# Kernel tuning notes

Measured on AMD Instinct MI355X. Metric: run time of the kernel, lower is better.

## Reference

```python
import jax, jax.numpy as jnp
import numpy as np

B, S, D, L, R = 8, 128, 512, 512, 50  # batch, seq_len, input_dim, linear_dim, n_rel_labels


def _head_params(key, n_out):
    k1, k2, k3, k4 = jax.random.split(key, 4)
    s1 = 1.0 / np.sqrt(2 * D)
    s2 = 1.0 / np.sqrt(L)
    return (jax.random.uniform(k1, (2 * D, L), jnp.float32, -s1, s1),
            jax.random.uniform(k2, (L,), jnp.float32, -s1, s1),
            jax.random.uniform(k3, (L, n_out), jnp.float32, -s2, s2),
            jax.random.uniform(k4, (n_out,), jnp.float32, -s2, s2))


def setup_inputs() -> dict:
    key = jax.random.key(0)
    kx, ks, kh, kt, kl = jax.random.split(key, 5)
    x = jax.random.normal(kx, (B, S, D), jnp.float32)
    span = _head_params(ks, 1)
    h2h = _head_params(kh, 1)
    t2t = _head_params(kt, 1)
    lab = _head_params(kl, R)
    return {
        'x': x,
        'span_W1': span[0], 'span_b1': span[1], 'span_W2': span[2], 'span_b2': span[3],
        'h2h_W1': h2h[0], 'h2h_b1': h2h[1], 'h2h_W2': h2h[2], 'h2h_b2': h2h[3],
        't2t_W1': t2t[0], 't2t_b1': t2t[1], 't2t_W2': t2t[2], 't2t_b2': t2t[3],
        'lab_W1': lab[0], 'lab_b1': lab[1], 'lab_W2': lab[2], 'lab_b2': lab[3],
    }


def _pair_head(x, W1, b1, W2, b2):
    # Linear on concat([x_i, x_j]) == x_i @ W_left + x_j @ W_right  (avoids [B,S,S,2D] concat)
    d = x.shape[-1]
    Wl, Wr = W1[:d], W1[d:]
    left = jnp.einsum('bid,dl->bil', x, Wl)   # [B,S,L]
    right = jnp.einsum('bjd,dl->bjl', x, Wr)  # [B,S,L]
    h = jnp.tanh(left[:, :, None, :] + right[:, None, :, :] + b1)  # [B,S,S,L]
    return jnp.einsum('bijl,lo->bijo', h, W2) + b2  # [B,S,S,n_out]


def reference(x, span_W1, span_b1, span_W2, span_b2,
              h2h_W1, h2h_b1, h2h_W2, h2h_b2,
              t2t_W1, t2t_b1, t2t_W2, t2t_b2,
              lab_W1, lab_b1, lab_W2, lab_b2):
    shst = _pair_head(x, span_W1, span_b1, span_W2, span_b2)[..., 0]  # [B,S,S]
    # torch: movedim(-1,1) -> triu + triu(1).T -> movedim(1,-1)
    bt = jnp.swapaxes(shst, 1, 2)
    sym = jnp.triu(bt) + jnp.swapaxes(jnp.triu(bt, 1), -1, -2)
    shst = jnp.swapaxes(sym, 1, 2)
    shoh = _pair_head(x, h2h_W1, h2h_b1, h2h_W2, h2h_b2)[..., 0]
    stot = _pair_head(x, t2t_W1, t2t_b1, t2t_W2, t2t_b2)[..., 0]
    shoh_labels = _pair_head(x, lab_W1, lab_b1, lab_W2, lab_b2)  # [B,S,S,R]
    return (shst, shoh, stot, shoh_labels)
```

## Files before the change

kernel.cpp:

```cpp
#include <hip/hip_runtime.h>

#define Bsz 8
#define Ssz 128
#define Dsz 512
#define D2 1024
#define Lsz 512
#define Rsz 50
#define SLOT 524288
#define BSLOT 65536
#define OUTMAT 131072

typedef __attribute__((ext_vector_type(8))) _Float16 f16x8;
typedef __attribute__((ext_vector_type(2))) __fp16 fp16x2;
typedef __attribute__((ext_vector_type(4))) float f32x4;

union UV4 { uint4 u; f16x8 h; };
union UH { unsigned short s; _Float16 h; };
union UP { fp16x2 h; unsigned u; };

struct K1Args {
  const float* W1[4];
  const float* b1[4];
};

__device__ __forceinline__ float f16lo(unsigned u) {
  UH x; x.s = (unsigned short)(u & 0xffffu); return (float)x.h;
}
__device__ __forceinline__ float f16hi(unsigned u) {
  UH x; x.s = (unsigned short)(u >> 16); return (float)x.h;
}
__device__ __forceinline__ unsigned pkrtz(float a, float b) {
  UP c; c.h = __builtin_amdgcn_cvt_pkrtz(a, b); return c.u;
}
__device__ __forceinline__ unsigned short f2h(float v) {
  UH x; x.h = (_Float16)v; return x.s;
}
__device__ __forceinline__ float rcpf(float x) {
  return __builtin_amdgcn_rcpf(x);
}

__global__ __launch_bounds__(256) void prep_all(
    const float* __restrict__ x, K1Args a, const float* __restrict__ W2,
    unsigned short* __restrict__ W1F, unsigned short* __restrict__ X16F,
    unsigned short* __restrict__ W2F) {
  const int z = blockIdx.z;
  const int t = threadIdx.x;
  if (z < 4) {
    if (blockIdx.x >= 8) return;
    __shared__ float S[64][65];
    const float* __restrict__ W = a.W1[z];
    const int n0 = blockIdx.x * 64;
    const int k0 = blockIdx.y * 64;
    {
      const int kk = t >> 2, c16 = (t & 3) * 16;
      const float* p = W + (k0 + kk) * Lsz + n0 + c16;
#pragma unroll
      for (int c = 0; c < 4; ++c) {
        float4 v = *(const float4*)(p + c * 4);
        S[kk][c16 + c * 4 + 0] = v.x; S[kk][c16 + c * 4 + 1] = v.y;
        S[kk][c16 + c * 4 + 2] = v.z; S[kk][c16 + c * 4 + 3] = v.w;
      }
    }
    __syncthreads();
#pragma unroll
    for (int o = t; o < 512; o += 256) {
      const int lane = o & 63;
      const int ntl = (o >> 6) & 3, kbl = o >> 8;
      const int n_l = ntl * 16 + (lane & 15);
      const int k_l = kbl * 32 + (lane >> 4) * 8;
      uint4 pk;
      pk.x = pkrtz(S[k_l + 0][n_l], S[k_l + 1][n_l]);
      pk.y = pkrtz(S[k_l + 2][n_l], S[k_l + 3][n_l]);
      pk.z = pkrtz(S[k_l + 4][n_l], S[k_l + 5][n_l]);
      pk.w = pkrtz(S[k_l + 6][n_l], S[k_l + 7][n_l]);
      const long addr =
          ((long)((z * 32 + blockIdx.x * 4 + ntl) * 32 + blockIdx.y * 2 + kbl) *
               64 + lane) * 8;
      *(uint4*)(W1F + addr) = pk;
    }
  } else if (z == 4) {
    const int idx = (blockIdx.y * 16 + blockIdx.x) * 256 + t;
    const int frag = idx >> 6, lane = idx & 63;
    const int m = (frag >> 4) * 16 + (lane & 15);
    const int k0 = (frag & 15) * 32 + (lane >> 4) * 8;
    const float* p = x + m * Dsz + k0;
    float4 v0 = *(const float4*)p, v1 = *(const float4*)(p + 4);
    uint4 pk = make_uint4(pkrtz(v0.x, v0.y), pkrtz(v0.z, v0.w),
                          pkrtz(v1.x, v1.y), pkrtz(v1.z, v1.w));
    *(uint4*)(X16F + (long)idx * 8) = pk;
  } else {
    if (blockIdx.y != 0 || blockIdx.x >= 16) return;
    const int idx = blockIdx.x * 256 + t;
    const int frag = idx >> 6, lane = idx & 63;
    const int o = (frag >> 4) * 16 + (lane & 15);
    const int k0 = (frag & 15) * 32 + (lane >> 4) * 8;
    float v[8];
#pragma unroll
    for (int e = 0; e < 8; ++e)
      v[e] = (o < Rsz) ? W2[(k0 + e) * Rsz + o] : 0.0f;
    uint4 pk = make_uint4(pkrtz(v[0], v[1]), pkrtz(v[2], v[3]),
                          pkrtz(v[4], v[5]), pkrtz(v[6], v[7]));
    *(uint4*)(W2F + (long)idx * 8) = pk;
  }
}

__global__ __launch_bounds__(256) void gemm_lr_f16f(
    const unsigned short* __restrict__ X16F,
    const unsigned short* __restrict__ W1F, K1Args a,
    unsigned short* __restrict__ U) {
  const int side = blockIdx.z;
  const int h = side >> 1, r = side & 1;
  const float* __restrict__ bias = a.b1[h];
  const int tid = threadIdx.x;
  const int w = tid >> 6, lane = tid & 63;
  const int lm = lane & 15, q = lane >> 4;
  const int mtb = blockIdx.y * 4 + (w & 1) * 2;
  const int ntb = blockIdx.x * 4 + (w >> 1) * 2;

  f32x4 acc[2][2];
#pragma unroll
  for (int mt = 0; mt < 2; ++mt)
#pragma unroll
    for (int nt = 0; nt < 2; ++nt) {
      acc[mt][nt].x = 0.f; acc[mt][nt].y = 0.f;
      acc[mt][nt].z = 0.f; acc[mt][nt].w = 0.f;
    }

  for (int kb = 0; kb < 16; ++kb) {
    UV4 af[2], bf[2];
#pragma unroll
    for (int mt = 0; mt < 2; ++mt)
      af[mt].u = *(const uint4*)(X16F +
          ((long)((mtb + mt) * 16 + kb) * 64 + lane) * 8);
#pragma unroll
    for (int nt = 0; nt < 2; ++nt)
      bf[nt].u = *(const uint4*)(W1F +
          ((long)((h * 32 + ntb + nt) * 32 + r * 16 + kb) * 64 + lane) * 8);
#pragma unroll
    for (int mt = 0; mt < 2; ++mt)
#pragma unroll
      for (int nt = 0; nt < 2; ++nt)
        acc[mt][nt] = __builtin_amdgcn_mfma_f32_16x16x32_f16(
            af[mt].h, bf[nt].h, acc[mt][nt], 0, 0, 0);
  }

  unsigned short* slot = U + side * SLOT;
  if (h < 3) {
#pragma unroll
    for (int nt = 0; nt < 2; ++nt) {
      const int n_out = (ntb + nt) * 16 + lm;
      const float bb = (r == 0) ? bias[n_out] : 0.0f;
#pragma unroll
      for (int mt = 0; mt < 2; ++mt) {
        const int m0r = (mtb + mt) * 16 + q * 4;
        const float e0 = __expf(2.0f * (acc[mt][nt].x + bb));
        const float e1 = __expf(2.0f * (acc[mt][nt].y + bb));
        const float e2 = __expf(2.0f * (acc[mt][nt].z + bb));
        const float e3 = __expf(2.0f * (acc[mt][nt].w + bb));
        uint2 pr;
        pr.x = pkrtz(e0, e1);
        pr.y = pkrtz(e2, e3);
        const int bi = m0r >> 7, il = m0r & 127;
        *(uint2*)(slot + bi * BSLOT + n_out * Ssz + il) = pr;
      }
    }
  } else {
#pragma unroll
    for (int nt = 0; nt < 2; ++nt) {
      const int n_out = (ntb + nt) * 16 + lm;
      const float bb = (r == 0) ? bias[n_out] : 0.0f;
#pragma unroll
      for (int mt = 0; mt < 2; ++mt) {
#pragma unroll
        for (int reg = 0; reg < 4; ++reg) {
          const int m_out = (mtb + mt) * 16 + q * 4 + reg;
          float v;
          if (reg == 0) v = acc[mt][nt].x;
          else if (reg == 1) v = acc[mt][nt].y;
          else if (reg == 2) v = acc[mt][nt].z;
          else v = acc[mt][nt].w;
          slot[m_out * Lsz + n_out] = f2h(__expf(2.0f * (v + bb)));
        }
      }
    }
  }
}

__global__ __launch_bounds__(256) void pair_scalar5(
    const unsigned short* __restrict__ U,
    const float* __restrict__ w2a, const float* __restrict__ w2b,
    const float* __restrict__ w2c, float* __restrict__ P) {
  const int zh = blockIdx.z;
  const int h = zh >> 1, half = zh & 1;
  const int b = blockIdx.y;
  const int it = blockIdx.x >> 2, jt = blockIdx.x & 3;
  if (h == 0 && jt > it) return;
  const int i0 = it * 32, j0 = jt * 32;
  const int t = threadIdx.x;
  const int tj = t & 15, ti = t >> 4;

  const unsigned short* __restrict__ A  = U + (2 * h) * SLOT + b * BSLOT;
  const unsigned short* __restrict__ Bt = U + (2 * h + 1) * SLOT + b * BSLOT;
  const float* __restrict__ w2 = (h == 0) ? w2a : (h == 1 ? w2b : w2c);

  __shared__ unsigned short Ls[64][40];
  __shared__ unsigned short Rs[64][40];
  __shared__ float w2s[64];

  float acc00 = 0.f, acc01 = 0.f, acc10 = 0.f, acc11 = 0.f;
  const int sr = t >> 2;
  const int sc = (t & 3) * 8;
  const int lbase = half * 256;

  for (int lc = 0; lc < 256; lc += 64) {
    __syncthreads();
    const int gl = lbase + lc + sr;
    *(uint4*)&Ls[sr][sc] = *(const uint4*)(A + gl * Ssz + i0 + sc);
    *(uint4*)&Rs[sr][sc] = *(const uint4*)(Bt + gl * Ssz + j0 + sc);
    if (t < 64) w2s[t] = w2[lbase + lc + t];
    __syncthreads();
#pragma unroll 4
    for (int l = 0; l < 64; ++l) {
      const unsigned ua = *(const unsigned*)&Ls[l][ti * 2];
      const unsigned ub = *(const unsigned*)&Rs[l][tj * 2];
      const float ax = f16lo(ua), ay = f16hi(ua);
      const float bx = f16lo(ub), by = f16hi(ub);
      const float wv = w2s[l];
      acc00 = fmaf(wv, rcpf(fmaf(ax, bx, 1.0f)), acc00);
      acc01 = fmaf(wv, rcpf(fmaf(ax, by, 1.0f)), acc01);
      acc10 = fmaf(wv, rcpf(fmaf(ay, bx, 1.0f)), acc10);
      acc11 = fmaf(wv, rcpf(fmaf(ay, by, 1.0f)), acc11);
    }
  }

  float* Pp = P + ((long)(zh * Bsz + b)) * 16384;
  const int i = i0 + ti * 2, j = j0 + tj * 2;
  *(float2*)&Pp[(i + 0) * Ssz + j] = make_float2(acc00, acc01);
  *(float2*)&Pp[(i + 1) * Ssz + j] = make_float2(acc10, acc11);
}

__global__ __launch_bounds__(128) void combine_scalar(
    const float* __restrict__ P,
    const float* __restrict__ w2a, const float* __restrict__ w2b,
    const float* __restrict__ w2c,
    const float* __restrict__ b2a, const float* __restrict__ b2b,
    const float* __restrict__ b2c,
    float* __restrict__ out) {
  const int h = blockIdx.z;
  const int b = blockIdx.y;
  const int i = blockIdx.x;
  const int t = threadIdx.x;
  const float* __restrict__ w2 = (h == 0) ? w2a : (h == 1 ? w2b : w2c);
  const float bias = (h == 0) ? b2a[0] : (h == 1 ? b2b[0] : b2c[0]);

  __shared__ float red[128];
  float s = w2[t] + w2[t + 128] + w2[t + 256] + w2[t + 384];
  red[t] = s;
  __syncthreads();
  if (t < 64) red[t] += red[t + 64];
  __syncthreads();
  if (t < 32) red[t] += red[t + 32];
  __syncthreads();
  if (t < 16) red[t] += red[t + 16];
  __syncthreads();
  if (t < 8) red[t] += red[t + 8];
  __syncthreads();
  if (t < 4) red[t] += red[t + 4];
  __syncthreads();
  if (t < 2) red[t] += red[t + 2];
  __syncthreads();
  const float S = red[0] + red[1];

  const float* P0 = P + ((long)(h * 2 * Bsz + b)) * 16384;
  const float* P1 = P + ((long)((h * 2 + 1) * Bsz + b)) * 16384;
  int ii = i, jj = t;
  if (h == 0 && t > i) { ii = t; jj = i; }
  const float p = P0[ii * Ssz + jj] + P1[ii * Ssz + jj];
  out[h * OUTMAT + (b * Ssz + i) * Ssz + t] = S - 2.0f * p + bias;
}

__global__ __launch_bounds__(256) void pair_label7(
    const unsigned short* __restrict__ U,
    const unsigned short* __restrict__ W2F,
    const float* __restrict__ b2, float* __restrict__ out) {
  const int b = blockIdx.z;
  const int i = blockIdx.x;
  const int tid = threadIdx.x;
  const int w = tid >> 6, lane = tid & 63;
  const int lm = lane & 15, q = lane >> 4;
  const int jb = blockIdx.y * 64 + w * 16;

  const unsigned short* __restrict__ L0 = U + 6 * SLOT + (b * Ssz + i) * Lsz;
  const unsigned short* __restrict__ Rr = U + 7 * SLOT + (b * Ssz + jb + lm) * Lsz;
  float* out3 = out + 3 * OUTMAT;

  f32x4 acc[4];
#pragma unroll
  for (int nt = 0; nt < 4; ++nt) {
    acc[nt].x = 0.f; acc[nt].y = 0.f;
    acc[nt].z = 0.f; acc[nt].w = 0.f;
  }

  const int kq = q * 8;
  uint4 rc  = *(const uint4*)(Rr + kq);
  uint4 l0c = *(const uint4*)(L0 + kq);

#pragma unroll 1
  for (int kc = 0; kc < Lsz; kc += 32) {
    const int kn = ((kc + 32) & 511) + kq;
    uint4 rn  = *(const uint4*)(Rr + kn);
    uint4 l0n = *(const uint4*)(L0 + kn);
    UV4 bf[4];
    const int kb = kc >> 5;
#pragma unroll
    for (int nt = 0; nt < 4; ++nt)
      bf[nt].u = *(const uint4*)(W2F + ((long)(nt * 16 + kb) * 64 + lane) * 8);

    float rf[8] = {f16lo(rc.x), f16hi(rc.x), f16lo(rc.y), f16hi(rc.y),
                   f16lo(rc.z), f16hi(rc.z), f16lo(rc.w), f16hi(rc.w)};
    float a0[8] = {f16lo(l0c.x), f16hi(l0c.x), f16lo(l0c.y), f16hi(l0c.y),
                   f16lo(l0c.z), f16hi(l0c.z), f16lo(l0c.w), f16hi(l0c.w)};
    float h0[8];
#pragma unroll
    for (int e = 0; e < 8; ++e)
      h0[e] = fmaf(-2.0f, rcpf(fmaf(a0[e], rf[e], 1.0f)), 1.0f);
    UV4 A0;
    A0.u = make_uint4(pkrtz(h0[0], h0[1]), pkrtz(h0[2], h0[3]),
                      pkrtz(h0[4], h0[5]), pkrtz(h0[6], h0[7]));
#pragma unroll
    for (int nt = 0; nt < 4; ++nt)
      acc[nt] = __builtin_amdgcn_mfma_f32_16x16x32_f16(
          A0.h, bf[nt].h, acc[nt], 0, 0, 0);
    rc = rn; l0c = l0n;
  }

#pragma unroll
  for (int nt = 0; nt < 4; ++nt) {
    const int o = nt * 16 + lm;
    if (o >= Rsz) continue;
    const float bias = b2[o];
#pragma unroll
    for (int reg = 0; reg < 4; ++reg) {
      const int j = jb + q * 4 + reg;
      const long base = ((long)((b * Ssz + i) * Ssz) + j) * Rsz;
      float v;
      if (reg == 0) v = acc[nt].x;
      else if (reg == 1) v = acc[nt].y;
      else if (reg == 2) v = acc[nt].z;
      else v = acc[nt].w;
      out3[base + o] = v + bias;
    }
  }
}

extern "C" void kernel_launch(void* const* d_in, const int* in_sizes, int n_in,
                              void* d_out, int out_size, void* d_ws,
                              size_t ws_size, hipStream_t stream) {
  (void)in_sizes; (void)n_in; (void)out_size; (void)ws_size;
  const float* x = (const float*)d_in[0];
  K1Args a;
  a.W1[0] = (const float*)d_in[1];  a.b1[0] = (const float*)d_in[2];
  a.W1[1] = (const float*)d_in[5];  a.b1[1] = (const float*)d_in[6];
  a.W1[2] = (const float*)d_in[9];  a.b1[2] = (const float*)d_in[10];
  a.W1[3] = (const float*)d_in[13]; a.b1[3] = (const float*)d_in[14];
  const float* w2a = (const float*)d_in[3];
  const float* b2a = (const float*)d_in[4];
  const float* w2b = (const float*)d_in[7];
  const float* b2b = (const float*)d_in[8];
  const float* w2c = (const float*)d_in[11];
  const float* b2c = (const float*)d_in[12];
  const float* W2l = (const float*)d_in[15];
  const float* b2l = (const float*)d_in[16];
  float* out = (float*)d_out;

  unsigned short* U    = (unsigned short*)d_ws;
  unsigned short* W1F  = U + 8 * SLOT;
  unsigned short* X16F = U + 8 * SLOT + 4 * (Lsz * D2);
  unsigned short* W2F  = U + 8 * SLOT + 5 * (Lsz * D2);
  float* P = (float*)W1F;

  prep_all<<<dim3(16, 16, 6), 256, 0, stream>>>(x, a, W2l, W1F, X16F, W2F);
  gemm_lr_f16f<<<dim3(8, 16, 8), 256, 0, stream>>>(X16F, W1F, a, U);
  pair_scalar5<<<dim3(16, Bsz, 6), 256, 0, stream>>>(U, w2a, w2b, w2c, P);
  combine_scalar<<<dim3(Ssz, Bsz, 3), 128, 0, stream>>>(
      P, w2a, w2b, w2c, b2a, b2b, b2c, out);
  pair_label7<<<dim3(Ssz, 2, Bsz), 256, 0, stream>>>(U, W2F, b2l, out);
}
```

Measured before the change: 185.3 us.

## Stage right-operand and W2 fragments in double-buffered LDS for label head

The label pair kernel now has each block cover all 128 j positions for one (b,i) row instead of 64, with each wave computing two 16-row M tiles. The right-hand activations and the W2 fragments are loaded cooperatively into double-buffered shared memory, and the next chunk is prefetched while the current one is computed. The aim is to cut redundant global loads of W2 and R rows across waves and blocks. In exchange the grid has half as many blocks, LDS use and register pressure rise, and a barrier is added per k chunk.

```diff
diff --git a/kernel.cpp b/kernel.cpp
--- a/kernel.cpp
+++ b/kernel.cpp
@@ -279,59 +279,113 @@
   out[h * OUTMAT + (b * Ssz + i) * Ssz + t] = S - 2.0f * p + bias;
 }
 
-__global__ __launch_bounds__(256) void pair_label7(
+__global__ __launch_bounds__(256) void pair_label8(
     const unsigned short* __restrict__ U,
     const unsigned short* __restrict__ W2F,
     const float* __restrict__ b2, float* __restrict__ out) {
-  const int b = blockIdx.z;
+  const int b = blockIdx.y;
   const int i = blockIdx.x;
   const int tid = threadIdx.x;
   const int w = tid >> 6, lane = tid & 63;
   const int lm = lane & 15, q = lane >> 4;
-  const int jb = blockIdx.y * 64 + w * 16;
-
-  const unsigned short* __restrict__ L0 = U + 6 * SLOT + (b * Ssz + i) * Lsz;
-  const unsigned short* __restrict__ Rr = U + 7 * SLOT + (b * Ssz + jb + lm) * Lsz;
+  const int jb = w * 32;
+
+  const unsigned short* __restrict__ Lrow = U + 6 * SLOT + (b * Ssz + i) * Lsz;
+  const unsigned short* __restrict__ Rb0 = U + 7 * SLOT + (long)b * Ssz * Lsz;
   float* out3 = out + 3 * OUTMAT;
 
-  f32x4 acc[4];
-#pragma unroll
-  for (int nt = 0; nt < 4; ++nt) {
-    acc[nt].x = 0.f; acc[nt].y = 0.f;
-    acc[nt].z = 0.f; acc[nt].w = 0.f;
-  }
-
-  const int kq = q * 8;
-  uint4 rc  = *(const uint4*)(Rr + kq);
-  uint4 l0c = *(const uint4*)(L0 + kq);
+  __shared__ unsigned short Rs[2][128][68];
+  __shared__ unsigned short Bs[2][8][512];
+
+  const int sr = tid >> 1;
+  const int sh = (tid & 1) * 32;
+  const unsigned short* Rg = Rb0 + sr * Lsz + sh;
+  const int bfrag = tid >> 5;
+  const int bo = (tid & 31) * 16;
+  const int fragN = (bfrag & 3) * 16 + (bfrag >> 2);
+
+  f32x4 acc[2][4];
+#pragma unroll
+  for (int mt = 0; mt < 2; ++mt)
+#pragma unroll
+    for (int nt = 0; nt < 4; ++nt) {
+      acc[mt][nt].x = 0.f; acc[mt][nt].y = 0.f;
+      acc[mt][nt].z = 0.f; acc[mt][nt].w = 0.f;
+    }
+
+  uint4 rp0, rp1, rp2, rp3, bp0, bp1;
+  {
+    const unsigned short* p = Rg;
+    rp0 = *(const uint4*)(p);      rp1 = *(const uint4*)(p + 8);
+    rp2 = *(const uint4*)(p + 16); rp3 = *(const uint4*)(p + 24);
+    const unsigned short* bp = W2F + (long)fragN * 512 + bo;
+    bp0 = *(const uint4*)(bp);     bp1 = *(const uint4*)(bp + 8);
+  }
+  *(uint4*)&Rs[0][sr][sh + 0]  = rp0;
+  *(uint4*)&Rs[0][sr][sh + 8]  = rp1;
+  *(uint4*)&Rs[0][sr][sh + 16] = rp2;
+  *(uint4*)&Rs[0][sr][sh + 24] = rp3;
+  *(uint4*)&Bs[0][bfrag][bo]     = bp0;
+  *(uint4*)&Bs[0][bfrag][bo + 8] = bp1;
+  __syncthreads();
 
 #pragma unroll 1
-  for (int kc = 0; kc < Lsz; kc += 32) {
-    const int kn = ((kc + 32) & 511) + kq;
-    uint4 rn  = *(const uint4*)(Rr + kn);
-    uint4 l0n = *(const uint4*)(L0 + kn);
-    UV4 bf[4];
-    const int kb = kc >> 5;
-#pragma unroll
-    for (int nt = 0; nt < 4; ++nt)
-      bf[nt].u = *(const uint4*)(W2F + ((long)(nt * 16 + kb) * 64 + lane) * 8);
-
-    float rf[8] = {f16lo(rc.x), f16hi(rc.x), f16lo(rc.y), f16hi(rc.y),
-                   f16lo(rc.z), f16hi(rc.z), f16lo(rc.w), f16hi(rc.w)};
-    float a0[8] = {f16lo(l0c.x), f16hi(l0c.x), f16lo(l0c.y), f16hi(l0c.y),
-                   f16lo(l0c.z), f16hi(l0c.z), f16lo(l0c.w), f16hi(l0c.w)};
-    float h0[8];
-#pragma unroll
-    for (int e = 0; e < 8; ++e)
-      h0[e] = fmaf(-2.0f, rcpf(fmaf(a0[e], rf[e], 1.0f)), 1.0f);
-    UV4 A0;
-    A0.u = make_uint4(pkrtz(h0[0], h0[1]), pkrtz(h0[2], h0[3]),
-                      pkrtz(h0[4], h0[5]), pkrtz(h0[6], h0[7]));
-#pragma unroll
-    for (int nt = 0; nt < 4; ++nt)
-      acc[nt] = __builtin_amdgcn_mfma_f32_16x16x32_f16(
-          A0.h, bf[nt].h, acc[nt], 0, 0, 0);
-    rc = rn; l0c = l0n;
+  for (int c = 0; c < 8; ++c) {
+    const int buf = c & 1;
+    if (c < 7) {
+      const unsigned short* p = Rg + (c + 1) * 64;
+      rp0 = *(const uint4*)(p);      rp1 = *(const uint4*)(p + 8);
+      rp2 = *(const uint4*)(p + 16); rp3 = *(const uint4*)(p + 24);
+      const unsigned short* bp = W2F + (long)(fragN + (c + 1) * 2) * 512 + bo;
+      bp0 = *(const uint4*)(bp);     bp1 = *(const uint4*)(bp + 8);
+    }
+    const uint4 lf0 = *(const uint4*)(Lrow + c * 64 + q * 8);
+    const uint4 lf1 = *(const uint4*)(Lrow + c * 64 + 32 + q * 8);
+
+#pragma unroll
+    for (int kbl = 0; kbl < 2; ++kbl) {
+      const uint4 lf = kbl ? lf1 : lf0;
+      float ea[8];
+      ea[0] = f16lo(lf.x); ea[1] = f16hi(lf.x);
+      ea[2] = f16lo(lf.y); ea[3] = f16hi(lf.y);
+      ea[4] = f16lo(lf.z); ea[5] = f16hi(lf.z);
+      ea[6] = f16lo(lf.w); ea[7] = f16hi(lf.w);
+      UV4 bfr[4];
+#pragma unroll
+      for (int nt = 0; nt < 4; ++nt)
+        bfr[nt].u = *(const uint4*)&Bs[buf][kbl * 4 + nt][lane * 8];
+#pragma unroll
+      for (int mt = 0; mt < 2; ++mt) {
+        const uint4 rv =
+            *(const uint4*)&Rs[buf][jb + mt * 16 + lm][kbl * 32 + q * 8];
+        float eb[8];
+        eb[0] = f16lo(rv.x); eb[1] = f16hi(rv.x);
+        eb[2] = f16lo(rv.y); eb[3] = f16hi(rv.y);
+        eb[4] = f16lo(rv.z); eb[5] = f16hi(rv.z);
+        eb[6] = f16lo(rv.w); eb[7] = f16hi(rv.w);
+        float hh[8];
+#pragma unroll
+        for (int e = 0; e < 8; ++e)
+          hh[e] = fmaf(-2.0f, rcpf(fmaf(ea[e], eb[e], 1.0f)), 1.0f);
+        UV4 A;
+        A.u = make_uint4(pkrtz(hh[0], hh[1]), pkrtz(hh[2], hh[3]),
+                         pkrtz(hh[4], hh[5]), pkrtz(hh[6], hh[7]));
+#pragma unroll
+        for (int nt = 0; nt < 4; ++nt)
+          acc[mt][nt] = __builtin_amdgcn_mfma_f32_16x16x32_f16(
+              A.h, bfr[nt].h, acc[mt][nt], 0, 0, 0);
+      }
+    }
+    if (c < 7) {
+      const int nb = buf ^ 1;
+      *(uint4*)&Rs[nb][sr][sh + 0]  = rp0;
+      *(uint4*)&Rs[nb][sr][sh + 8]  = rp1;
+      *(uint4*)&Rs[nb][sr][sh + 16] = rp2;
+      *(uint4*)&Rs[nb][sr][sh + 24] = rp3;
+      *(uint4*)&Bs[nb][bfrag][bo]     = bp0;
+      *(uint4*)&Bs[nb][bfrag][bo + 8] = bp1;
+    }
+    __syncthreads();
   }
 
 #pragma unroll
@@ -340,15 +394,18 @@
     if (o >= Rsz) continue;
     const float bias = b2[o];
 #pragma unroll
-    for (int reg = 0; reg < 4; ++reg) {
-      const int j = jb + q * 4 + reg;
-      const long base = ((long)((b * Ssz + i) * Ssz) + j) * Rsz;
-      float v;
-      if (reg == 0) v = acc[nt].x;
-      else if (reg == 1) v = acc[nt].y;
-      else if (reg == 2) v = acc[nt].z;
-      else v = acc[nt].w;
-      out3[base + o] = v + bias;
+    for (int mt = 0; mt < 2; ++mt) {
+#pragma unroll
+      for (int reg = 0; reg < 4; ++reg) {
+        const int j = jb + mt * 16 + q * 4 + reg;
+        const long base = ((long)((b * Ssz + i) * Ssz) + j) * Rsz;
+        float v;
+        if (reg == 0) v = acc[mt][nt].x;
+        else if (reg == 1) v = acc[mt][nt].y;
+        else if (reg == 2) v = acc[mt][nt].z;
+        else v = acc[mt][nt].w;
+        out3[base + o] = v + bias;
+      }
     }
   }
 }
@@ -384,5 +441,5 @@
   pair_scalar5<<<dim3(16, Bsz, 6), 256, 0, stream>>>(U, w2a, w2b, w2c, P);
   combine_scalar<<<dim3(Ssz, Bsz, 3), 128, 0, stream>>>(
       P, w2a, w2b, w2c, b2a, b2b, b2c, out);
-  pair_label7<<<dim3(Ssz, 2, Bsz), 256, 0, stream>>>(U, W2F, b2l, out);
-}
+  pair_label8<<<dim3(Ssz, Bsz), 256, 0, stream>>>(U, W2F, b2l, out);
+}
```

After: 168.7 us. 9.0% less time.
